# Performance work log

Measured on AMD Instinct MI355X. Metric: run time of the kernel, lower is better.

## Reference

```python
import jax, jax.numpy as jnp
import numpy as np

EPS = 1e-8  # torch F.cosine_similarity norm clamp


def setup_inputs() -> dict:
    key = jax.random.key(0)
    ks = jax.random.split(key, 5)
    B, H, C, S, CS, K = 256, 256, 16384, 64, 32, 8
    query = jax.random.normal(ks[0], (B, H), dtype=jnp.float32)
    episode_embeddings = jax.random.normal(ks[1], (C, H), dtype=jnp.float32)
    episodes = jax.random.normal(ks[2], (C, S, H), dtype=jnp.float32)
    compressed_episodes = jax.random.normal(ks[3], (C, CS, H), dtype=jnp.float32)
    is_compressed = jax.random.randint(ks[4], (C,), 0, 2) == 1
    return {
        "query": query,
        "episode_embeddings": episode_embeddings,
        "episodes": episodes,
        "compressed_episodes": compressed_episodes,
        "is_compressed": is_compressed,
        "k": K,
    }


def reference(query, episode_embeddings, episodes, compressed_episodes, is_compressed, k):
    # cosine similarity  [B, C]
    qn = query / jnp.maximum(jnp.linalg.norm(query, axis=-1, keepdims=True), EPS)
    en = episode_embeddings / jnp.maximum(
        jnp.linalg.norm(episode_embeddings, axis=-1, keepdims=True), EPS)
    sim = qn @ en.T
    top_scores, top_idx = jax.lax.top_k(sim, k)  # [B, k]

    S = episodes.shape[1]
    CS = compressed_episodes.shape[1]
    full = episodes[top_idx]                # [B, k, S, H] gather
    comp = compressed_episodes[top_idx]     # [B, k, CS, H] gather
    comp_padded = jnp.pad(comp, ((0, 0), (0, 0), (0, S - CS), (0, 0)))
    flag = is_compressed[top_idx][..., None, None]  # [B, k, 1, 1]
    retrieved = jnp.where(flag, comp_padded, full)  # [B, k, S, H]
    return retrieved, top_scores
```

## Files before the change

kernel.cpp:

```cpp
#include <hip/hip_runtime.h>
#include <math.h>

#define B_  256
#define H_  256
#define C_  16384
#define S_  64
#define CS_ 32
#define K_  8
#define EPS 1e-8f
#define RET_ ((size_t)B_ * K_ * S_ * H_)

typedef __attribute__((ext_vector_type(8))) short short8v;
typedef __attribute__((ext_vector_type(4))) float f32x4;


__device__ inline unsigned short f2bf(float f) {
    unsigned u = __builtin_bit_cast(unsigned, f);
    unsigned r = u + 0x7fffu + ((u >> 16) & 1u);
    return (unsigned short)(r >> 16);
}
__device__ inline unsigned ordf(float f) {
    unsigned u = __builtin_bit_cast(unsigned, f);
    return u ^ ((u >> 31) ? 0xFFFFFFFFu : 0x80000000u);
}

#define LSTR 40
__global__ __launch_bounds__(256) void sim_mfma_kernel(const float* __restrict__ q,
                                                       const float* __restrict__ e,
                                                       float* __restrict__ sim) {
    __shared__ unsigned short Qs[64 * LSTR];
    __shared__ unsigned short Es[64 * LSTR];
    __shared__ float einv_s[64];
    const int t = threadIdx.x, lane = t & 63, wv = t >> 6;
    const int wm = wv >> 1, wn = wv & 1;
    const int c0 = blockIdx.x * 64, b0 = blockIdx.y * 64;
    const int srow = t >> 2, shg = t & 3;
    const float4* q4 = (const float4*)q;
    const float4* e4 = (const float4*)e;

    float esq = 0.f;
    f32x4 acc[2][2];
    #pragma unroll
    for (int i = 0; i < 2; ++i)
        #pragma unroll
        for (int j = 0; j < 2; ++j) acc[i][j] = (f32x4){0.f, 0.f, 0.f, 0.f};

    for (int hc = 0; hc < 8; ++hc) {
        __syncthreads();
        float4 a0 = q4[(size_t)(b0 + srow) * 64 + hc * 8 + shg * 2];
        float4 a1 = q4[(size_t)(b0 + srow) * 64 + hc * 8 + shg * 2 + 1];
        float4 e0 = e4[(size_t)(c0 + srow) * 64 + hc * 8 + shg * 2];
        float4 e1 = e4[(size_t)(c0 + srow) * 64 + hc * 8 + shg * 2 + 1];
        esq += e0.x * e0.x + e0.y * e0.y + e0.z * e0.z + e0.w * e0.w
             + e1.x * e1.x + e1.y * e1.y + e1.z * e1.z + e1.w * e1.w;
        short8v qa, ea;
        qa[0] = (short)f2bf(a0.x); qa[1] = (short)f2bf(a0.y);
        qa[2] = (short)f2bf(a0.z); qa[3] = (short)f2bf(a0.w);
        qa[4] = (short)f2bf(a1.x); qa[5] = (short)f2bf(a1.y);
        qa[6] = (short)f2bf(a1.z); qa[7] = (short)f2bf(a1.w);
        ea[0] = (short)f2bf(e0.x); ea[1] = (short)f2bf(e0.y);
        ea[2] = (short)f2bf(e0.z); ea[3] = (short)f2bf(e0.w);
        ea[4] = (short)f2bf(e1.x); ea[5] = (short)f2bf(e1.y);
        ea[6] = (short)f2bf(e1.z); ea[7] = (short)f2bf(e1.w);
        *(short8v*)&Qs[srow * LSTR + shg * 8] = qa;
        *(short8v*)&Es[srow * LSTR + shg * 8] = ea;
        __syncthreads();

        short8v afr[2], bfr[2];
        #pragma unroll
        for (int mi = 0; mi < 2; ++mi)
            afr[mi] = *(short8v*)&Qs[(wm * 32 + mi * 16 + (lane & 15)) * LSTR + (lane >> 4) * 8];
        #pragma unroll
        for (int ni = 0; ni < 2; ++ni)
            bfr[ni] = *(short8v*)&Es[(wn * 32 + ni * 16 + (lane & 15)) * LSTR + (lane >> 4) * 8];
        #pragma unroll
        for (int mi = 0; mi < 2; ++mi)
            #pragma unroll
            for (int ni = 0; ni < 2; ++ni)
                acc[mi][ni] = __builtin_amdgcn_mfma_f32_16x16x32_bf16(
                    afr[mi], bfr[ni], acc[mi][ni], 0, 0, 0);
    }

    esq += __shfl_xor(esq, 1);
    esq += __shfl_xor(esq, 2);
    if (shg == 0) einv_s[srow] = 1.0f / fmaxf(sqrtf(esq), EPS);
    __syncthreads();

    #pragma unroll
    for (int mi = 0; mi < 2; ++mi) {
        #pragma unroll
        for (int j = 0; j < 4; ++j) {
            int b = b0 + wm * 32 + mi * 16 + (lane >> 4) * 4 + j;
            #pragma unroll
            for (int ni = 0; ni < 2; ++ni) {
                int cc = wn * 32 + ni * 16 + (lane & 15);
                sim[(size_t)b * C_ + c0 + cc] = acc[mi][ni][j] * einv_s[cc];
            }
        }
    }
}

__global__ __launch_bounds__(256) void select_kernel(const float* __restrict__ q,
                                                     const float* __restrict__ e,
                                                     const float* __restrict__ sim,
                                                     const unsigned* __restrict__ icw,
                                                     int* __restrict__ mode,
                                                     float* __restrict__ out_scores,
                                                     int* __restrict__ top_idx) {
    const int t = threadIdx.x, b = blockIdx.x;
    if (b == 256) {
        __shared__ int f;
        if (t == 0) f = 0;
        __syncthreads();
        int any = 0;
        for (int i = t; i < 4096; i += 256)
            if (icw[i] & 0xFFFFFF00u) any = 1;
        if (any) atomicOr(&f, 1);
        __syncthreads();
        if (t == 0) *mode = f;
        return;
    }

    __shared__ unsigned long long keys[1024];
    __shared__ float rs[32];
    __shared__ int   ri[32];
    const float* row = sim + (size_t)b * C_;

    float s[4]; int id[4];
    #pragma unroll
    for (int k = 0; k < 4; ++k) { s[k] = -INFINITY; id[k] = 0x7fffffff; }
    for (int i = 0; i < 64; ++i) {
        int c = i * 256 + t;
        float v = row[c];
        if (v > s[3] || (v == s[3] && c < id[3])) {
            s[3] = v; id[3] = c;
            #pragma unroll
            for (int k = 3; k > 0; --k) {
                if (s[k] > s[k-1] || (s[k] == s[k-1] && id[k] < id[k-1])) {
                    float tv = s[k]; s[k] = s[k-1]; s[k-1] = tv;
                    int ti = id[k]; id[k] = id[k-1]; id[k-1] = ti;
                }
            }
        }
    }
    #pragma unroll
    for (int k = 0; k < 4; ++k)
        keys[t * 4 + k] = ((unsigned long long)ordf(s[k]) << 32)
                        | (unsigned)(0xFFFFFFFFu - (unsigned)id[k]);
    __syncthreads();

    for (int k = 2; k <= 1024; k <<= 1) {
        for (int j = k >> 1; j > 0; j >>= 1) {
            #pragma unroll
            for (int base = 0; base < 1024; base += 256) {
                int i = base + t, l = i ^ j;
                if (l > i) {
                    unsigned long long a = keys[i], bb = keys[l];
                    bool up = ((i & k) == 0);
                    if ((a > bb) == up) { keys[i] = bb; keys[l] = a; }
                }
            }
            __syncthreads();
        }
    }

    const int wv = t >> 6, lane = t & 63;
    float4 qv = ((const float4*)q)[(size_t)b * 64 + lane];
    float qsq = qv.x * qv.x + qv.y * qv.y + qv.z * qv.z + qv.w * qv.w;
    #pragma unroll
    for (int d = 1; d < 64; d <<= 1) qsq += __shfl_xor(qsq, d);
    float qi = 1.0f / fmaxf(sqrtf(qsq), EPS);

    for (int m = wv; m < 32; m += 4) {
        unsigned long long key = keys[1023 - m];
        int idx = (int)(0xFFFFFFFFu - (unsigned)(key & 0xFFFFFFFFull));
        float4 ev = ((const float4*)e)[(size_t)idx * 64 + lane];
        float dot = qv.x * ev.x + qv.y * ev.y + qv.z * ev.z + qv.w * ev.w;
        float ss  = ev.x * ev.x + ev.y * ev.y + ev.z * ev.z + ev.w * ev.w;
        #pragma unroll
        for (int d = 1; d < 64; d <<= 1) {
            dot += __shfl_xor(dot, d);
            ss  += __shfl_xor(ss, d);
        }
        if (lane == 0) {
            rs[m] = dot * qi * (1.0f / fmaxf(sqrtf(ss), EPS));
            ri[m] = idx;
        }
    }
    __syncthreads();

    if (t < 64) {
        float val; int idx, slot;
        if (t < 32) { val = rs[t]; idx = ri[t]; slot = t; }
        else        { val = -INFINITY; idx = 0x7fffffff; slot = -1; }
        for (int p = 0; p < 8; ++p) {
            float bs = val; int bi = idx, bsl = slot;
            #pragma unroll
            for (int d = 1; d < 64; d <<= 1) {
                float os = __shfl_xor(bs, d);
                int   oi = __shfl_xor(bi, d);
                int   osl = __shfl_xor(bsl, d);
                if (os > bs || (os == bs && oi < bi)) { bs = os; bi = oi; bsl = osl; }
            }
            if (t == 0) { out_scores[b * K_ + p] = bs; top_idx[b * K_ + p] = bi; }
            if (slot == bsl) val = -INFINITY;
        }
    }
}

__global__ __launch_bounds__(256) void gather_kernel(const float* __restrict__ epi,
                                                     const float* __restrict__ comp,
                                                     const void* __restrict__ icp,
                                                     const int* __restrict__ top_idx,
                                                     const int* __restrict__ mode,
                                                     float* __restrict__ out) {
    const int bj = blockIdx.x;
    const int c = top_idx[bj];
    const int m = *mode;
    const int flag = m ? (((const unsigned char*)icp)[c] != 0)
                       : (((const int*)icp)[c] != 0);
    f32x4* o4 = (f32x4*)out + (size_t)bj * 4096;
    if (!flag) {
        const f32x4* s4 = (const f32x4*)epi + (size_t)c * 4096;
        #pragma unroll 4
        for (int i = threadIdx.x; i < 4096; i += 256)
            __builtin_nontemporal_store(__builtin_nontemporal_load(s4 + i), o4 + i);
    } else {
        const f32x4* s4 = (const f32x4*)comp + (size_t)c * 2048;
        #pragma unroll 4
        for (int i = threadIdx.x; i < 2048; i += 256)
            __builtin_nontemporal_store(__builtin_nontemporal_load(s4 + i), o4 + i);
        const f32x4 z = (f32x4){0.f, 0.f, 0.f, 0.f};
        #pragma unroll 4
        for (int i = 2048 + threadIdx.x; i < 4096; i += 256)
            __builtin_nontemporal_store(z, o4 + i);
    }
}

extern "C" void kernel_launch(void* const* d_in, const int* in_sizes, int n_in,
                              void* d_out, int out_size, void* d_ws, size_t ws_size,
                              hipStream_t stream) {
    const float* query = (const float*)d_in[0];
    const float* emb   = (const float*)d_in[1];
    const float* epi   = (const float*)d_in[2];
    const float* comp  = (const float*)d_in[3];
    const void*  icp   = d_in[4];
    float* out = (float*)d_out;

    int* mode   = (int*)d_ws;
    int* topidx = mode + 1;

    float* simbuf     = out;
    float* out_scores = out + RET_;

    sim_mfma_kernel<<<dim3(C_ / 64, B_ / 64), 256, 0, stream>>>(query, emb, simbuf);
    select_kernel<<<257, 256, 0, stream>>>(query, emb, simbuf, (const unsigned*)icp,
                                           mode, out_scores, topidx);
    gather_kernel<<<B_ * K_, 256, 0, stream>>>(epi, comp, icp, topidx, mode, out);
}
```

Baseline: 125.2 us.

## Fuse similarity GEMM with per-tile top-8 selection and merge candidates

The similarity kernel now stages the full 256-wide H slice of Q and E tiles in shared memory once and computes the 64x64 tile without per-chunk syncs. Each tile then picks a local top-8 per query row and writes packed keys to a candidate buffer, so the full 256x16384 similarity matrix is never written to global memory. A merge kernel bitonic-sorts the 2048 candidates per row instead of scanning 16384 floats. Block indices are remapped to group column tiles. The larger shared-memory footprint may lower occupancy, and the merge sort is twice as long.

```diff
diff --git a/kernel.cpp b/kernel.cpp
--- a/kernel.cpp
+++ b/kernel.cpp
@@ -23,56 +23,67 @@
     unsigned u = __builtin_bit_cast(unsigned, f);
     return u ^ ((u >> 31) ? 0xFFFFFFFFu : 0x80000000u);
 }
-
-#define LSTR 40
-__global__ __launch_bounds__(256) void sim_mfma_kernel(const float* __restrict__ q,
-                                                       const float* __restrict__ e,
-                                                       float* __restrict__ sim) {
-    __shared__ unsigned short Qs[64 * LSTR];
-    __shared__ unsigned short Es[64 * LSTR];
+__device__ inline short8v pack8(float4 a, float4 b) {
+    short8v r;
+    r[0] = (short)f2bf(a.x); r[1] = (short)f2bf(a.y);
+    r[2] = (short)f2bf(a.z); r[3] = (short)f2bf(a.w);
+    r[4] = (short)f2bf(b.x); r[5] = (short)f2bf(b.y);
+    r[6] = (short)f2bf(b.z); r[7] = (short)f2bf(b.w);
+    return r;
+}
+
+#define LSTR 264
+__global__ __launch_bounds__(256) void simsel_kernel(const float* __restrict__ q,
+                                                     const float* __restrict__ e,
+                                                     unsigned long long* __restrict__ candbuf) {
+    __shared__ union {
+        struct { unsigned short Qs[64 * LSTR]; unsigned short Es[64 * LSTR]; } st;
+        float tile[64 * 65];
+    } sm;
     __shared__ float einv_s[64];
     const int t = threadIdx.x, lane = t & 63, wv = t >> 6;
     const int wm = wv >> 1, wn = wv & 1;
-    const int c0 = blockIdx.x * 64, b0 = blockIdx.y * 64;
-    const int srow = t >> 2, shg = t & 3;
+    const int bid = blockIdx.x;
+    const int ct = (bid & 7) * 32 + ((bid >> 3) >> 2);
+    const int bt = (bid >> 3) & 3;
+    const int c0 = ct * 64, b0 = bt * 64;
+    const int r = t >> 2, g = t & 3;
     const float4* q4 = (const float4*)q;
     const float4* e4 = (const float4*)e;
 
     float esq = 0.f;
-    f32x4 acc[2][2];
-    #pragma unroll
-    for (int i = 0; i < 2; ++i)
-        #pragma unroll
-        for (int j = 0; j < 2; ++j) acc[i][j] = (f32x4){0.f, 0.f, 0.f, 0.f};
-
-    for (int hc = 0; hc < 8; ++hc) {
-        __syncthreads();
-        float4 a0 = q4[(size_t)(b0 + srow) * 64 + hc * 8 + shg * 2];
-        float4 a1 = q4[(size_t)(b0 + srow) * 64 + hc * 8 + shg * 2 + 1];
-        float4 e0 = e4[(size_t)(c0 + srow) * 64 + hc * 8 + shg * 2];
-        float4 e1 = e4[(size_t)(c0 + srow) * 64 + hc * 8 + shg * 2 + 1];
+    #pragma unroll
+    for (int u = 0; u < 16; u += 2) {
+        float4 a0 = q4[(size_t)(b0 + r) * 64 + g * 16 + u];
+        float4 a1 = q4[(size_t)(b0 + r) * 64 + g * 16 + u + 1];
+        *(short8v*)&sm.st.Qs[r * LSTR + g * 64 + u * 4] = pack8(a0, a1);
+        float4 e0 = e4[(size_t)(c0 + r) * 64 + g * 16 + u];
+        float4 e1 = e4[(size_t)(c0 + r) * 64 + g * 16 + u + 1];
         esq += e0.x * e0.x + e0.y * e0.y + e0.z * e0.z + e0.w * e0.w
              + e1.x * e1.x + e1.y * e1.y + e1.z * e1.z + e1.w * e1.w;
-        short8v qa, ea;
-        qa[0] = (short)f2bf(a0.x); qa[1] = (short)f2bf(a0.y);
-        qa[2] = (short)f2bf(a0.z); qa[3] = (short)f2bf(a0.w);
-        qa[4] = (short)f2bf(a1.x); qa[5] = (short)f2bf(a1.y);
-        qa[6] = (short)f2bf(a1.z); qa[7] = (short)f2bf(a1.w);
-        ea[0] = (short)f2bf(e0.x); ea[1] = (short)f2bf(e0.y);
-        ea[2] = (short)f2bf(e0.z); ea[3] = (short)f2bf(e0.w);
-        ea[4] = (short)f2bf(e1.x); ea[5] = (short)f2bf(e1.y);
-        ea[6] = (short)f2bf(e1.z); ea[7] = (short)f2bf(e1.w);
-        *(short8v*)&Qs[srow * LSTR + shg * 8] = qa;
-        *(short8v*)&Es[srow * LSTR + shg * 8] = ea;
-        __syncthreads();
-
+        *(short8v*)&sm.st.Es[r * LSTR + g * 64 + u * 4] = pack8(e0, e1);
+    }
+    esq += __shfl_xor(esq, 1);
+    esq += __shfl_xor(esq, 2);
+    if (g == 0) einv_s[r] = 1.0f / fmaxf(sqrtf(esq), EPS);
+    __syncthreads();
+
+    f32x4 acc[2][2];
+    #pragma unroll
+    for (int i = 0; i < 2; ++i)
+        #pragma unroll
+        for (int j = 0; j < 2; ++j) acc[i][j] = (f32x4){0.f, 0.f, 0.f, 0.f};
+    #pragma unroll
+    for (int hc = 0; hc < 8; ++hc) {
         short8v afr[2], bfr[2];
         #pragma unroll
         for (int mi = 0; mi < 2; ++mi)
-            afr[mi] = *(short8v*)&Qs[(wm * 32 + mi * 16 + (lane & 15)) * LSTR + (lane >> 4) * 8];
+            afr[mi] = *(short8v*)&sm.st.Qs[(wm * 32 + mi * 16 + (lane & 15)) * LSTR
+                                           + hc * 32 + (lane >> 4) * 8];
         #pragma unroll
         for (int ni = 0; ni < 2; ++ni)
-            bfr[ni] = *(short8v*)&Es[(wn * 32 + ni * 16 + (lane & 15)) * LSTR + (lane >> 4) * 8];
+            bfr[ni] = *(short8v*)&sm.st.Es[(wn * 32 + ni * 16 + (lane & 15)) * LSTR
+                                           + hc * 32 + (lane >> 4) * 8];
         #pragma unroll
         for (int mi = 0; mi < 2; ++mi)
             #pragma unroll
@@ -80,33 +91,52 @@
                 acc[mi][ni] = __builtin_amdgcn_mfma_f32_16x16x32_bf16(
                     afr[mi], bfr[ni], acc[mi][ni], 0, 0, 0);
     }
-
-    esq += __shfl_xor(esq, 1);
-    esq += __shfl_xor(esq, 2);
-    if (shg == 0) einv_s[srow] = 1.0f / fmaxf(sqrtf(esq), EPS);
-    __syncthreads();
-
-    #pragma unroll
-    for (int mi = 0; mi < 2; ++mi) {
+    __syncthreads();
+
+    #pragma unroll
+    for (int mi = 0; mi < 2; ++mi)
         #pragma unroll
         for (int j = 0; j < 4; ++j) {
-            int b = b0 + wm * 32 + mi * 16 + (lane >> 4) * 4 + j;
+            int row = wm * 32 + mi * 16 + (lane >> 4) * 4 + j;
             #pragma unroll
             for (int ni = 0; ni < 2; ++ni) {
-                int cc = wn * 32 + ni * 16 + (lane & 15);
-                sim[(size_t)b * C_ + c0 + cc] = acc[mi][ni][j] * einv_s[cc];
-            }
-        }
-    }
-}
-
-__global__ __launch_bounds__(256) void select_kernel(const float* __restrict__ q,
-                                                     const float* __restrict__ e,
-                                                     const float* __restrict__ sim,
-                                                     const unsigned* __restrict__ icw,
-                                                     int* __restrict__ mode,
-                                                     float* __restrict__ out_scores,
-                                                     int* __restrict__ top_idx) {
+                int col = wn * 32 + ni * 16 + (lane & 15);
+                sm.tile[row * 65 + col] = acc[mi][ni][j] * einv_s[col];
+            }
+        }
+    __syncthreads();
+
+    if (t < 64) {
+        unsigned long long best[8];
+        #pragma unroll
+        for (int k = 0; k < 8; ++k) best[k] = 0ull;
+        for (int c = 0; c < 64; ++c) {
+            float v = sm.tile[t * 65 + c];
+            unsigned long long key = ((unsigned long long)ordf(v) << 32)
+                                   | (unsigned)(0xFFFFFFFFu - (unsigned)(c0 + c));
+            if (key > best[7]) {
+                best[7] = key;
+                #pragma unroll
+                for (int k = 7; k > 0; --k)
+                    if (best[k] > best[k - 1]) {
+                        unsigned long long tmp = best[k];
+                        best[k] = best[k - 1]; best[k - 1] = tmp;
+                    }
+            }
+        }
+        #pragma unroll
+        for (int k = 0; k < 8; ++k)
+            candbuf[(size_t)(b0 + t) * 2048 + ct * 8 + k] = best[k];
+    }
+}
+
+__global__ __launch_bounds__(256) void merge_kernel(const float* __restrict__ q,
+                                                    const float* __restrict__ e,
+                                                    const unsigned long long* __restrict__ candbuf,
+                                                    const unsigned* __restrict__ icw,
+                                                    int* __restrict__ mode,
+                                                    float* __restrict__ out_scores,
+                                                    int* __restrict__ top_idx) {
     const int t = threadIdx.x, b = blockIdx.x;
     if (b == 256) {
         __shared__ int f;
@@ -121,38 +151,18 @@
         return;
     }
 
-    __shared__ unsigned long long keys[1024];
+    __shared__ unsigned long long keys[2048];
     __shared__ float rs[32];
     __shared__ int   ri[32];
-    const float* row = sim + (size_t)b * C_;
-
-    float s[4]; int id[4];
-    #pragma unroll
-    for (int k = 0; k < 4; ++k) { s[k] = -INFINITY; id[k] = 0x7fffffff; }
-    for (int i = 0; i < 64; ++i) {
-        int c = i * 256 + t;
-        float v = row[c];
-        if (v > s[3] || (v == s[3] && c < id[3])) {
-            s[3] = v; id[3] = c;
-            #pragma unroll
-            for (int k = 3; k > 0; --k) {
-                if (s[k] > s[k-1] || (s[k] == s[k-1] && id[k] < id[k-1])) {
-                    float tv = s[k]; s[k] = s[k-1]; s[k-1] = tv;
-                    int ti = id[k]; id[k] = id[k-1]; id[k-1] = ti;
-                }
-            }
-        }
-    }
-    #pragma unroll
-    for (int k = 0; k < 4; ++k)
-        keys[t * 4 + k] = ((unsigned long long)ordf(s[k]) << 32)
-                        | (unsigned)(0xFFFFFFFFu - (unsigned)id[k]);
-    __syncthreads();
-
-    for (int k = 2; k <= 1024; k <<= 1) {
+    const unsigned long long* row = candbuf + (size_t)b * 2048;
+    #pragma unroll
+    for (int k = 0; k < 8; ++k) keys[t * 8 + k] = row[t * 8 + k];
+    __syncthreads();
+
+    for (int k = 2; k <= 2048; k <<= 1) {
         for (int j = k >> 1; j > 0; j >>= 1) {
             #pragma unroll
-            for (int base = 0; base < 1024; base += 256) {
+            for (int base = 0; base < 2048; base += 256) {
                 int i = base + t, l = i ^ j;
                 if (l > i) {
                     unsigned long long a = keys[i], bb = keys[l];
@@ -172,7 +182,7 @@
     float qi = 1.0f / fmaxf(sqrtf(qsq), EPS);
 
     for (int m = wv; m < 32; m += 4) {
-        unsigned long long key = keys[1023 - m];
+        unsigned long long key = keys[2047 - m];
         int idx = (int)(0xFFFFFFFFu - (unsigned)(key & 0xFFFFFFFFull));
         float4 ev = ((const float4*)e)[(size_t)idx * 64 + lane];
         float dot = qv.x * ev.x + qv.y * ev.y + qv.z * ev.z + qv.w * ev.w;
@@ -247,14 +257,13 @@
     const void*  icp   = d_in[4];
     float* out = (float*)d_out;
 
-    int* mode   = (int*)d_ws;
+    unsigned long long* candbuf = (unsigned long long*)d_ws;
+    int* mode   = (int*)((char*)d_ws + (4u << 20));
     int* topidx = mode + 1;
-
-    float* simbuf     = out;
     float* out_scores = out + RET_;
 
-    sim_mfma_kernel<<<dim3(C_ / 64, B_ / 64), 256, 0, stream>>>(query, emb, simbuf);
-    select_kernel<<<257, 256, 0, stream>>>(query, emb, simbuf, (const unsigned*)icp,
-                                           mode, out_scores, topidx);
+    simsel_kernel<<<1024, 256, 0, stream>>>(query, emb, candbuf);
+    merge_kernel<<<257, 256, 0, stream>>>(query, emb, candbuf, (const unsigned*)icp,
+                                          mode, out_scores, topidx);
     gather_kernel<<<B_ * K_, 256, 0, stream>>>(epi, comp, icp, topidx, mode, out);
 }
```

Result: slower. 150.6 us (+20.3%).
